# Kernel tuning notes

Hardware: AMD Instinct MI355X
Metric: run time of the kernel (lower is better)

Reference implementation:

```python
import jax, jax.numpy as jnp
import numpy as np

B, N, D_IN, E, H = 4, 512, 256, 64, 4
NEG = 1.0e9


def setup_inputs() -> dict:
    key = jax.random.key(0)
    ks = jax.random.split(key, 7)
    s = 1.0 / np.sqrt(D_IN)  # dense-init scale
    return {
        "x": jax.random.normal(ks[0], (B, N, D_IN), jnp.float32),
        "Wq": jax.random.normal(ks[1], (H, D_IN, E), jnp.float32) * s,
        "bq": jnp.zeros((H, E), jnp.float32),
        "Wk": jax.random.normal(ks[2], (H, D_IN, E), jnp.float32) * s,
        "bk": jnp.zeros((H, E), jnp.float32),
        "Wv": jax.random.normal(ks[3], (H, D_IN, E), jnp.float32) * s,
        "bv": jnp.zeros((H, E), jnp.float32),
    }


def _sdp(q, k, v):
    logits = jnp.einsum('bne,bme->bnm', q, k) / jnp.sqrt(jnp.asarray(E, q.dtype))
    return jnp.einsum('bnm,bme->bne', jax.nn.softmax(logits, axis=-1), v)


def _cosine(q, k, v):
    qn = q / jnp.linalg.norm(q, axis=-1, keepdims=True)
    kn = k / jnp.linalg.norm(k, axis=-1, keepdims=True)
    logits = jnp.einsum('bne,bme->bnm', qn, kn)
    return jnp.einsum('bnm,bme->bne', jax.nn.softmax(logits, axis=-1), v)


def _l1(q, k, v):
    # [B,N,N] L1 distances via broadcasted [B,N,N,E] diff, as in the original
    d = jnp.sum(jnp.abs(q[:, :, None, :] - k[:, None, :, :]), axis=-1)
    return jnp.einsum('bnm,bme->bne', jax.nn.softmax(-d, axis=-1), v)


def _l2(q, k, v):
    d = jnp.sqrt(jnp.sum(jnp.square(q[:, :, None, :] - k[:, None, :, :]), axis=-1))
    return jnp.einsum('bnm,bme->bne', jax.nn.softmax(-d, axis=-1), v)


_HEAD_FNS = (_sdp, _cosine, _l1, _l2)  # attention_types per head


def reference(x, Wq, bq, Wk, bk, Wv, bv):
    # Per-head projections: [B,H,N,E]
    q = jnp.einsum('bnd,hde->bhne', x, Wq) + bq[None, :, None, :]
    k = jnp.einsum('bnd,hde->bhne', x, Wk) + bk[None, :, None, :]
    v = jnp.einsum('bnd,hde->bhne', x, Wv) + bv[None, :, None, :]
    outs = [fn(q[:, h], k[:, h], v[:, h]) for h, fn in enumerate(_HEAD_FNS)]
    return jnp.concatenate(outs, axis=-1)  # [B,N,H*E]
```

## Files before the change

kernel.cpp:

```cpp
#include <hip/hip_runtime.h>
#include <hip/hip_bf16.h>
#include <math.h>

#define B_   4
#define N_   512
#define DIN  256
#define E_   64
#define H_   4

typedef __attribute__((ext_vector_type(8))) short bf16x8;
typedef __attribute__((ext_vector_type(4))) float f32x4;

__device__ __forceinline__ unsigned short f2bf(float f) {
    __hip_bfloat16 h = __float2bfloat16(f);
    return *reinterpret_cast<unsigned short*>(&h);
}

__global__ __launch_bounds__(256) void proj_kernel(
    const float* __restrict__ x,
    const float* __restrict__ Wq, const float* __restrict__ bq,
    const float* __restrict__ Wk, const float* __restrict__ bk,
    const float* __restrict__ Wv, const float* __restrict__ bv,
    float* __restrict__ Q, float* __restrict__ KT,
    float* __restrict__ qn2, float* __restrict__ kn2,
    unsigned short* __restrict__ Qp, unsigned short* __restrict__ Kp,
    unsigned short* __restrict__ VTp)
{
    const int tid = threadIdx.x;
    int blk = blockIdx.x;
    const int tile = blk & 15;  blk >>= 4;
    const int p    = blk % 3;   blk /= 3;
    const int h    = blk & 3;
    const int b    = blk >> 2;

    const float* W;
    const float* bias;
    if (p == 0)      { W = Wq; bias = bq; }
    else if (p == 1) { W = Wk; bias = bk; }
    else             { W = Wv; bias = bv; }
    W    += (size_t)h * DIN * E_;
    bias += h * E_;

    const int rowbase = tile * 32;
    const float* xb = x + ((size_t)b * N_ + rowbase) * DIN;

    __shared__ float XsT[64][34];
    __shared__ float Ws[64][64];
    __shared__ float Ys[64][33];

    const int tr = tid >> 4;
    const int tc = tid & 15;

    float acc[2][4];
    #pragma unroll
    for (int i = 0; i < 2; ++i)
        #pragma unroll
        for (int j = 0; j < 4; ++j) acc[i][j] = 0.f;

    for (int dc = 0; dc < DIN; dc += 64) {
        for (int l = tid; l < 2048; l += 256) {
            int r = l >> 6, d = l & 63;
            XsT[d][r] = xb[r * DIN + dc + d];
        }
        {
            const float4* Wg4 = (const float4*)(W + (size_t)dc * E_);
            #pragma unroll
            for (int i = 0; i < 4; ++i) ((float4*)Ws)[tid + i * 256] = Wg4[tid + i * 256];
        }
        __syncthreads();

        #pragma unroll 8
        for (int d = 0; d < 64; ++d) {
            float2 xv = *(const float2*)&XsT[d][tr * 2];
            float4 wv = *(const float4*)&Ws[d][tc * 4];
            acc[0][0] = fmaf(xv.x, wv.x, acc[0][0]);
            acc[0][1] = fmaf(xv.x, wv.y, acc[0][1]);
            acc[0][2] = fmaf(xv.x, wv.z, acc[0][2]);
            acc[0][3] = fmaf(xv.x, wv.w, acc[0][3]);
            acc[1][0] = fmaf(xv.y, wv.x, acc[1][0]);
            acc[1][1] = fmaf(xv.y, wv.y, acc[1][1]);
            acc[1][2] = fmaf(xv.y, wv.z, acc[1][2]);
            acc[1][3] = fmaf(xv.y, wv.w, acc[1][3]);
        }
        __syncthreads();
    }

    const size_t bh = (size_t)b * H_ + h;
    float4 bias4 = *(const float4*)&bias[tc * 4];
    float v0[4], v1[4];
    v0[0] = acc[0][0] + bias4.x; v0[1] = acc[0][1] + bias4.y;
    v0[2] = acc[0][2] + bias4.z; v0[3] = acc[0][3] + bias4.w;
    v1[0] = acc[1][0] + bias4.x; v1[1] = acc[1][1] + bias4.y;
    v1[2] = acc[1][2] + bias4.z; v1[3] = acc[1][3] + bias4.w;

    const int r0 = rowbase + tr * 2;

    if (p < 2) {
        float s0 = 0.f, s1 = 0.f;
        #pragma unroll
        for (int j = 0; j < 4; ++j) {
            s0 = fmaf(v0[j], v0[j], s0);
            s1 = fmaf(v1[j], v1[j], s1);
        }
        #pragma unroll
        for (int off = 1; off < 16; off <<= 1) {
            s0 += __shfl_xor(s0, off, 64);
            s1 += __shfl_xor(s1, off, 64);
        }
        if (tc == 0) {
            float* nrm = (p == 0) ? qn2 : kn2;
            nrm[bh * N_ + r0]     = s0;
            nrm[bh * N_ + r0 + 1] = s1;
        }
        unsigned short* pk = ((p == 0) ? Qp : Kp) + bh * (size_t)(N_ * E_);
        ushort4 u0, u1;
        u0.x = f2bf(v0[0]); u0.y = f2bf(v0[1]); u0.z = f2bf(v0[2]); u0.w = f2bf(v0[3]);
        u1.x = f2bf(v1[0]); u1.y = f2bf(v1[1]); u1.z = f2bf(v1[2]); u1.w = f2bf(v1[3]);
        *(ushort4*)&pk[(size_t)r0 * E_ + tc * 4]       = u0;
        *(ushort4*)&pk[(size_t)(r0 + 1) * E_ + tc * 4] = u1;
    }

    if (p == 0) {
        float* o = Q + bh * (size_t)(N_ * E_);
        *(float4*)&o[(size_t)r0 * E_ + tc * 4]       = make_float4(v0[0], v0[1], v0[2], v0[3]);
        *(float4*)&o[(size_t)(r0 + 1) * E_ + tc * 4] = make_float4(v1[0], v1[1], v1[2], v1[3]);
    } else {
        #pragma unroll
        for (int j = 0; j < 4; ++j) {
            Ys[tc * 4 + j][tr * 2]     = v0[j];
            Ys[tc * 4 + j][tr * 2 + 1] = v1[j];
        }
        __syncthreads();
        const int e  = tid >> 2;
        const int n0 = (tid & 3) * 8;
        if (p == 1) {
            float* o = KT + bh * (size_t)(E_ * N_) + (size_t)e * N_ + rowbase + n0;
            float4 a, c;
            a.x = Ys[e][n0 + 0]; a.y = Ys[e][n0 + 1];
            a.z = Ys[e][n0 + 2]; a.w = Ys[e][n0 + 3];
            c.x = Ys[e][n0 + 4]; c.y = Ys[e][n0 + 5];
            c.z = Ys[e][n0 + 6]; c.w = Ys[e][n0 + 7];
            *(float4*)&o[0] = a;
            *(float4*)&o[4] = c;
        } else {
            unsigned short* o = VTp + bh * (size_t)(E_ * N_) + (size_t)e * N_ + rowbase + n0;
            ushort4 a, c;
            a.x = f2bf(Ys[e][n0 + 0]); a.y = f2bf(Ys[e][n0 + 1]);
            a.z = f2bf(Ys[e][n0 + 2]); a.w = f2bf(Ys[e][n0 + 3]);
            c.x = f2bf(Ys[e][n0 + 4]); c.y = f2bf(Ys[e][n0 + 5]);
            c.z = f2bf(Ys[e][n0 + 6]); c.w = f2bf(Ys[e][n0 + 7]);
            *(ushort4*)&o[0] = a;
            *(ushort4*)&o[4] = c;
        }
    }
}

template <int HEAD>
__device__ __forceinline__ void mfma_logits(
    int w, int lane, size_t bh, int q0,
    const unsigned short* __restrict__ Qp,
    const unsigned short* __restrict__ Kp,
    const float* __restrict__ qn2, const float* __restrict__ kn2,
    char* Pw, float (*wmax)[16], float (*wsum)[16])
{
    const int g = lane >> 4, li = lane & 15;
    const int row0 = g * 4;
    const unsigned short* Qpb = Qp + bh * (N_ * E_) + (size_t)q0 * E_;
    const unsigned short* Kpb = Kp + bh * (N_ * E_);

    bf16x8 a0 = *(const bf16x8*)&Qpb[li * E_ + g * 8];
    bf16x8 a1 = *(const bf16x8*)&Qpb[li * E_ + g * 8 + 32];

    float qrow[4];
    if (HEAD == 1) {
        #pragma unroll
        for (int j = 0; j < 4; ++j) qrow[j] = rsqrtf(qn2[bh * N_ + q0 + row0 + j]);
    } else if (HEAD == 3) {
        #pragma unroll
        for (int j = 0; j < 4; ++j) qrow[j] = qn2[bh * N_ + q0 + row0 + j];
    }

    float lg[8][4];
    #pragma unroll
    for (int t = 0; t < 8; ++t) {
        const int m0 = w * 128 + t * 16;
        const unsigned short* kb = &Kpb[(size_t)(m0 + li) * E_ + g * 8];
        bf16x8 b0 = *(const bf16x8*)&kb[0];
        bf16x8 b1 = *(const bf16x8*)&kb[32];
        f32x4 acc = {0.f, 0.f, 0.f, 0.f};
        acc = __builtin_amdgcn_mfma_f32_16x16x32_bf16(a0, b0, acc, 0, 0, 0);
        acc = __builtin_amdgcn_mfma_f32_16x16x32_bf16(a1, b1, acc, 0, 0, 0);
        float kcol = 0.f, rk = 0.f;
        if (HEAD == 1) { kcol = kn2[bh * N_ + m0 + li]; rk = rsqrtf(kcol); }
        if (HEAD == 3) { kcol = kn2[bh * N_ + m0 + li]; }
        #pragma unroll
        for (int j = 0; j < 4; ++j) {
            float d = acc[j];
            if (HEAD == 0)      lg[t][j] = d * 0.125f;
            else if (HEAD == 1) lg[t][j] = d * qrow[j] * rk;
            else                lg[t][j] = -sqrtf(fmaxf(qrow[j] + kcol - 2.f * d, 0.f));
        }
    }

    float mx[4], gm[4];
    #pragma unroll
    for (int j = 0; j < 4; ++j) {
        float m = lg[0][j];
        #pragma unroll
        for (int t = 1; t < 8; ++t) m = fmaxf(m, lg[t][j]);
        #pragma unroll
        for (int off = 1; off < 16; off <<= 1) m = fmaxf(m, __shfl_xor(m, off, 64));
        mx[j] = m;
    }
    if (li == 0) {
        #pragma unroll
        for (int j = 0; j < 4; ++j) wmax[w][row0 + j] = mx[j];
    }
    __syncthreads();
    #pragma unroll
    for (int j = 0; j < 4; ++j)
        gm[j] = fmaxf(fmaxf(wmax[0][row0 + j], wmax[1][row0 + j]),
                      fmaxf(wmax[2][row0 + j], wmax[3][row0 + j]));

    float sm[4] = {0.f, 0.f, 0.f, 0.f};
    #pragma unroll
    for (int t = 0; t < 8; ++t) {
        #pragma unroll
        for (int j = 0; j < 4; ++j) {
            const int row = row0 + j;
            float pv = __expf(lg[t][j] - gm[j]);
            sm[j] += pv;
            const int byte = (row * 256 + (t * 16 + li) * 2) ^ ((row & 7) << 4);
            *(unsigned short*)(Pw + byte) = f2bf(pv);
        }
    }
    #pragma unroll
    for (int j = 0; j < 4; ++j) {
        float s = sm[j];
        #pragma unroll
        for (int off = 1; off < 16; off <<= 1) s += __shfl_xor(s, off, 64);
        if (li == 0) wsum[w][row0 + j] = s;
    }
}

__global__ __launch_bounds__(256) void attn_kernel(
    const float* __restrict__ Qf, const float* __restrict__ KT,
    const unsigned short* __restrict__ Qp, const unsigned short* __restrict__ Kp,
    const unsigned short* __restrict__ VTp,
    const float* __restrict__ qn2, const float* __restrict__ kn2,
    float* __restrict__ out)
{
    const int tid  = threadIdx.x;
    const int w    = tid >> 6;
    const int lane = tid & 63;
    int blk = blockIdx.x;
    const int qt = blk & 31;
    const int h  = (blk >> 5) & 3;
    const int b  = blk >> 7;
    const size_t bh = (size_t)b * H_ + h;
    const int q0 = qt * 16;

    __shared__ unsigned short Plds[4][2048];
    __shared__ float part[4][16][68];
    __shared__ float wmax[4][16];
    __shared__ float wsum[4][16];
    __shared__ float q_lds[16][72];

    const int g = lane >> 4, li = lane & 15;
    char* Pw = (char*)&Plds[w][0];

    if (h == 2) {
        {
            const int i4 = tid * 4;
            const int r = i4 >> 6, c = i4 & 63;
            *(float4*)&q_lds[r][c] =
                *(const float4*)&Qf[bh * (N_ * E_) + (size_t)(q0 + r) * E_ + c];
        }
        __syncthreads();

        float acc0[16], acc1[16];
        #pragma unroll
        for (int r = 0; r < 16; ++r) { acc0[r] = 0.f; acc1[r] = 0.f; }

        const float* kp = KT + bh * (E_ * N_) + w * 128 + 2 * lane;
        for (int c = 0; c < 4; ++c) {
            float2 kk[16];
            #pragma unroll
            for (int i = 0; i < 16; ++i) kk[i] = *(const float2*)&kp[(c * 16 + i) * N_];
            #pragma unroll
            for (int r = 0; r < 16; ++r) {
                const float* qr = &q_lds[r][c * 16];
                float4 qa = *(const float4*)&qr[0];
                float4 qb = *(const float4*)&qr[4];
                float4 qc = *(const float4*)&qr[8];
                float4 qd = *(const float4*)&qr[12];
                float qv[16] = {qa.x, qa.y, qa.z, qa.w, qb.x, qb.y, qb.z, qb.w,
                                qc.x, qc.y, qc.z, qc.w, qd.x, qd.y, qd.z, qd.w};
                #pragma unroll
                for (int i = 0; i < 16; ++i) {
                    acc0[r] += fabsf(kk[i].x - qv[i]);
                    acc1[r] += fabsf(kk[i].y - qv[i]);
                }
            }
        }

        #pragma unroll
        for (int r = 0; r < 16; ++r) {
            float mn = fminf(acc0[r], acc1[r]);
            #pragma unroll
            for (int off = 1; off < 64; off <<= 1) mn = fminf(mn, __shfl_xor(mn, off, 64));
            if (lane == 0) wmax[w][r] = mn;
        }
        __syncthreads();
        #pragma unroll
        for (int r = 0; r < 16; ++r) {
            float gmn = fminf(fminf(wmax[0][r], wmax[1][r]), fminf(wmax[2][r], wmax[3][r]));
            float p0 = __expf(gmn - acc0[r]);
            float p1 = __expf(gmn - acc1[r]);
            float s = p0 + p1;
            #pragma unroll
            for (int off = 1; off < 64; off <<= 1) s += __shfl_xor(s, off, 64);
            if (lane == 0) wsum[w][r] = s;
            unsigned int pk = (unsigned int)f2bf(p0) | ((unsigned int)f2bf(p1) << 16);
            const int byte = (r * 256 + lane * 4) ^ ((r & 7) << 4);
            *(unsigned int*)(Pw + byte) = pk;
        }
    } else if (h == 0) {
        mfma_logits<0>(w, lane, bh, q0, Qp, Kp, qn2, kn2, Pw, wmax, wsum);
    } else if (h == 1) {
        mfma_logits<1>(w, lane, bh, q0, Qp, Kp, qn2, kn2, Pw, wmax, wsum);
    } else {
        mfma_logits<3>(w, lane, bh, q0, Qp, Kp, qn2, kn2, Pw, wmax, wsum);
    }

    {
        bf16x8 pa[4];
        #pragma unroll
        for (int s = 0; s < 4; ++s) {
            const int byte = (li * 256 + (s * 32 + g * 8) * 2) ^ ((li & 7) << 4);
            pa[s] = *(const bf16x8*)(Pw + byte);
        }
        const unsigned short* Vb = VTp + bh * (E_ * N_);
        const int row0 = g * 4;
        #pragma unroll
        for (int et = 0; et < 4; ++et) {
            f32x4 acc = {0.f, 0.f, 0.f, 0.f};
            #pragma unroll
            for (int s = 0; s < 4; ++s) {
                bf16x8 vb = *(const bf16x8*)&Vb[(size_t)(et * 16 + li) * N_
                                                + w * 128 + s * 32 + g * 8];
                acc = __builtin_amdgcn_mfma_f32_16x16x32_bf16(pa[s], vb, acc, 0, 0, 0);
            }
            #pragma unroll
            for (int j = 0; j < 4; ++j) part[w][row0 + j][et * 16 + li] = acc[j];
        }
    }
    __syncthreads();

    #pragma unroll
    for (int k = 0; k < 4; ++k) {
        const int idx = tid + k * 256;
        const int row = idx >> 6, e = idx & 63;
        float s = part[0][row][e] + part[1][row][e] + part[2][row][e] + part[3][row][e];
        float rs = wsum[0][row] + wsum[1][row] + wsum[2][row] + wsum[3][row];
        out[((size_t)b * N_ + q0 + row) * (H_ * E_) + h * E_ + e] = s / rs;
    }
}

extern "C" void kernel_launch(void* const* d_in, const int* in_sizes, int n_in,
                              void* d_out, int out_size, void* d_ws, size_t ws_size,
                              hipStream_t stream)
{
    const float* x  = (const float*)d_in[0];
    const float* Wq = (const float*)d_in[1];
    const float* bq = (const float*)d_in[2];
    const float* Wk = (const float*)d_in[3];
    const float* bk = (const float*)d_in[4];
    const float* Wv = (const float*)d_in[5];
    const float* bv = (const float*)d_in[6];
    float* out = (float*)d_out;

    const size_t qkv = (size_t)B_ * H_ * N_ * E_;
    float* Q   = (float*)d_ws;
    float* KT  = Q + qkv;
    float* qn2 = KT + qkv;
    float* kn2 = qn2 + (size_t)B_ * H_ * N_;
    unsigned short* Qp  = (unsigned short*)(kn2 + (size_t)B_ * H_ * N_);
    unsigned short* Kp  = Qp + qkv;
    unsigned short* VTp = Kp + qkv;

    proj_kernel<<<B_ * H_ * 3 * (N_ / 32), 256, 0, stream>>>(
        x, Wq, bq, Wk, bk, Wv, bv, Q, KT, qn2, kn2, Qp, Kp, VTp);
    attn_kernel<<<B_ * H_ * (N_ / 16), 256, 0, stream>>>(
        Q, KT, Qp, Kp, VTp, qn2, kn2, out);
}
```

Baseline: 58.97 us.

## Double attention block to eight waves with shared P tile and split PV

The attention kernel now runs 512 threads per block, eight waves, each handling 64 keys instead of 128. The probability tile is stored as one shared 16x512 LDS buffer instead of per-wave slices. The PV product is redistributed so each wave computes one 16-column output tile over half the keys, which cuts the cross-wave reduction to two partials. This halves per-thread work on the L1 head and the logits, aiming to shorten the critical path and hide latency. The cost is an extra block-wide barrier and more LDS per block, which may lower occupancy.

```diff
diff --git a/kernel.cpp b/kernel.cpp
--- a/kernel.cpp
+++ b/kernel.cpp
@@ -155,13 +155,15 @@
     }
 }
 
+#define PROW 1024
+
 template <int HEAD>
 __device__ __forceinline__ void mfma_logits(
     int w, int lane, size_t bh, int q0,
     const unsigned short* __restrict__ Qp,
     const unsigned short* __restrict__ Kp,
     const float* __restrict__ qn2, const float* __restrict__ kn2,
-    char* Pw, float (*wmax)[16], float (*wsum)[16])
+    char* Pb, float (*wmax)[16], float (*wsum)[16])
 {
     const int g = lane >> 4, li = lane & 15;
     const int row0 = g * 4;
@@ -180,10 +182,10 @@
         for (int j = 0; j < 4; ++j) qrow[j] = qn2[bh * N_ + q0 + row0 + j];
     }
 
-    float lg[8][4];
-    #pragma unroll
-    for (int t = 0; t < 8; ++t) {
-        const int m0 = w * 128 + t * 16;
+    float lg[4][4];
+    #pragma unroll
+    for (int t = 0; t < 4; ++t) {
+        const int m0 = w * 64 + t * 16;
         const unsigned short* kb = &Kpb[(size_t)(m0 + li) * E_ + g * 8];
         bf16x8 b0 = *(const bf16x8*)&kb[0];
         bf16x8 b1 = *(const bf16x8*)&kb[32];
@@ -202,12 +204,12 @@
         }
     }
 
-    float mx[4], gm[4];
+    float mx[4];
     #pragma unroll
     for (int j = 0; j < 4; ++j) {
         float m = lg[0][j];
         #pragma unroll
-        for (int t = 1; t < 8; ++t) m = fmaxf(m, lg[t][j]);
+        for (int t = 1; t < 4; ++t) m = fmaxf(m, lg[t][j]);
         #pragma unroll
         for (int off = 1; off < 16; off <<= 1) m = fmaxf(m, __shfl_xor(m, off, 64));
         mx[j] = m;
@@ -217,21 +219,27 @@
         for (int j = 0; j < 4; ++j) wmax[w][row0 + j] = mx[j];
     }
     __syncthreads();
-    #pragma unroll
-    for (int j = 0; j < 4; ++j)
-        gm[j] = fmaxf(fmaxf(wmax[0][row0 + j], wmax[1][row0 + j]),
-                      fmaxf(wmax[2][row0 + j], wmax[3][row0 + j]));
+
+    float gm[4];
+    #pragma unroll
+    for (int j = 0; j < 4; ++j) {
+        float m = wmax[0][row0 + j];
+        #pragma unroll
+        for (int ww = 1; ww < 8; ++ww) m = fmaxf(m, wmax[ww][row0 + j]);
+        gm[j] = m;
+    }
 
     float sm[4] = {0.f, 0.f, 0.f, 0.f};
     #pragma unroll
-    for (int t = 0; t < 8; ++t) {
+    for (int t = 0; t < 4; ++t) {
         #pragma unroll
         for (int j = 0; j < 4; ++j) {
             const int row = row0 + j;
+            const int key = w * 64 + t * 16 + li;
             float pv = __expf(lg[t][j] - gm[j]);
             sm[j] += pv;
-            const int byte = (row * 256 + (t * 16 + li) * 2) ^ ((row & 7) << 4);
-            *(unsigned short*)(Pw + byte) = f2bf(pv);
+            const int byte = (row * PROW + key * 2) ^ ((row & 7) << 4);
+            *(unsigned short*)(Pb + byte) = f2bf(pv);
         }
     }
     #pragma unroll
@@ -243,7 +251,7 @@
     }
 }
 
-__global__ __launch_bounds__(256) void attn_kernel(
+__global__ __launch_bounds__(512) void attn_kernel(
     const float* __restrict__ Qf, const float* __restrict__ KT,
     const unsigned short* __restrict__ Qp, const unsigned short* __restrict__ Kp,
     const unsigned short* __restrict__ VTp,
@@ -260,33 +268,34 @@
     const size_t bh = (size_t)b * H_ + h;
     const int q0 = qt * 16;
 
-    __shared__ unsigned short Plds[4][2048];
-    __shared__ float part[4][16][68];
-    __shared__ float wmax[4][16];
-    __shared__ float wsum[4][16];
+    __shared__ unsigned short Plds[16 * 512];
+    __shared__ float part[2][16][68];
+    __shared__ float wmax[8][16];
+    __shared__ float wsum[8][16];
     __shared__ float q_lds[16][72];
 
     const int g = lane >> 4, li = lane & 15;
-    char* Pw = (char*)&Plds[w][0];
+    char* Pb = (char*)Plds;
 
     if (h == 2) {
-        {
-            const int i4 = tid * 4;
-            const int r = i4 >> 6, c = i4 & 63;
+        if (tid < 256) {
+            const int r = tid >> 4, c = (tid & 15) * 4;
             *(float4*)&q_lds[r][c] =
                 *(const float4*)&Qf[bh * (N_ * E_) + (size_t)(q0 + r) * E_ + c];
         }
         __syncthreads();
 
-        float acc0[16], acc1[16];
-        #pragma unroll
-        for (int r = 0; r < 16; ++r) { acc0[r] = 0.f; acc1[r] = 0.f; }
-
-        const float* kp = KT + bh * (E_ * N_) + w * 128 + 2 * lane;
+        const int n = w * 64 + lane;
+        const float* kp = KT + bh * (E_ * N_) + n;
+        float acc[16];
+        #pragma unroll
+        for (int r = 0; r < 16; ++r) acc[r] = 0.f;
+
+        #pragma unroll
         for (int c = 0; c < 4; ++c) {
-            float2 kk[16];
-            #pragma unroll
-            for (int i = 0; i < 16; ++i) kk[i] = *(const float2*)&kp[(c * 16 + i) * N_];
+            float kk[16];
+            #pragma unroll
+            for (int i = 0; i < 16; ++i) kk[i] = kp[(size_t)(c * 16 + i) * N_];
             #pragma unroll
             for (int r = 0; r < 16; ++r) {
                 const float* qr = &q_lds[r][c * 16];
@@ -297,72 +306,67 @@
                 float qv[16] = {qa.x, qa.y, qa.z, qa.w, qb.x, qb.y, qb.z, qb.w,
                                 qc.x, qc.y, qc.z, qc.w, qd.x, qd.y, qd.z, qd.w};
                 #pragma unroll
-                for (int i = 0; i < 16; ++i) {
-                    acc0[r] += fabsf(kk[i].x - qv[i]);
-                    acc1[r] += fabsf(kk[i].y - qv[i]);
-                }
+                for (int i = 0; i < 16; ++i) acc[r] += fabsf(kk[i] - qv[i]);
             }
         }
 
         #pragma unroll
         for (int r = 0; r < 16; ++r) {
-            float mn = fminf(acc0[r], acc1[r]);
+            float mn = acc[r];
             #pragma unroll
             for (int off = 1; off < 64; off <<= 1) mn = fminf(mn, __shfl_xor(mn, off, 64));
             if (lane == 0) wmax[w][r] = mn;
         }
         __syncthreads();
+
         #pragma unroll
         for (int r = 0; r < 16; ++r) {
-            float gmn = fminf(fminf(wmax[0][r], wmax[1][r]), fminf(wmax[2][r], wmax[3][r]));
-            float p0 = __expf(gmn - acc0[r]);
-            float p1 = __expf(gmn - acc1[r]);
-            float s = p0 + p1;
+            float gmn = wmax[0][r];
+            #pragma unroll
+            for (int ww = 1; ww < 8; ++ww) gmn = fminf(gmn, wmax[ww][r]);
+            float p = __expf(gmn - acc[r]);
+            float s = p;
             #pragma unroll
             for (int off = 1; off < 64; off <<= 1) s += __shfl_xor(s, off, 64);
             if (lane == 0) wsum[w][r] = s;
-            unsigned int pk = (unsigned int)f2bf(p0) | ((unsigned int)f2bf(p1) << 16);
-            const int byte = (r * 256 + lane * 4) ^ ((r & 7) << 4);
-            *(unsigned int*)(Pw + byte) = pk;
+            const int byte = (r * PROW + n * 2) ^ ((r & 7) << 4);
+            *(unsigned short*)(Pb + byte) = f2bf(p);
         }
     } else if (h == 0) {
-        mfma_logits<0>(w, lane, bh, q0, Qp, Kp, qn2, kn2, Pw, wmax, wsum);
+        mfma_logits<0>(w, lane, bh, q0, Qp, Kp, qn2, kn2, Pb, wmax, wsum);
     } else if (h == 1) {
-        mfma_logits<1>(w, lane, bh, q0, Qp, Kp, qn2, kn2, Pw, wmax, wsum);
+        mfma_logits<1>(w, lane, bh, q0, Qp, Kp, qn2, kn2, Pb, wmax, wsum);
     } else {
-        mfma_logits<3>(w, lane, bh, q0, Qp, Kp, qn2, kn2, Pw, wmax, wsum);
-    }
+        mfma_logits<3>(w, lane, bh, q0, Qp, Kp, qn2, kn2, Pb, wmax, wsum);
+    }
+    __syncthreads();
 
     {
-        bf16x8 pa[4];
-        #pragma unroll
-        for (int s = 0; s < 4; ++s) {
-            const int byte = (li * 256 + (s * 32 + g * 8) * 2) ^ ((li & 7) << 4);
-            pa[s] = *(const bf16x8*)(Pw + byte);
-        }
-        const unsigned short* Vb = VTp + bh * (E_ * N_);
-        const int row0 = g * 4;
-        #pragma unroll
-        for (int et = 0; et < 4; ++et) {
-            f32x4 acc = {0.f, 0.f, 0.f, 0.f};
-            #pragma unroll
-            for (int s = 0; s < 4; ++s) {
-                bf16x8 vb = *(const bf16x8*)&Vb[(size_t)(et * 16 + li) * N_
-                                                + w * 128 + s * 32 + g * 8];
-                acc = __builtin_amdgcn_mfma_f32_16x16x32_bf16(pa[s], vb, acc, 0, 0, 0);
-            }
-            #pragma unroll
-            for (int j = 0; j < 4; ++j) part[w][row0 + j][et * 16 + li] = acc[j];
-        }
+        const int et = w & 3, kh = w >> 2;
+        f32x4 acc = {0.f, 0.f, 0.f, 0.f};
+        const unsigned short* Vb = VTp + bh * (E_ * N_)
+                                 + (size_t)(et * 16 + li) * N_ + kh * 256;
+        #pragma unroll
+        for (int s = 0; s < 8; ++s) {
+            const int byte = (li * PROW + (kh * 256 + s * 32 + g * 8) * 2)
+                           ^ ((li & 7) << 4);
+            bf16x8 pa = *(const bf16x8*)(Pb + byte);
+            bf16x8 vb = *(const bf16x8*)&Vb[s * 32 + g * 8];
+            acc = __builtin_amdgcn_mfma_f32_16x16x32_bf16(pa, vb, acc, 0, 0, 0);
+        }
+        #pragma unroll
+        for (int j = 0; j < 4; ++j) part[kh][g * 4 + j][et * 16 + li] = acc[j];
     }
     __syncthreads();
 
     #pragma unroll
-    for (int k = 0; k < 4; ++k) {
-        const int idx = tid + k * 256;
+    for (int k = 0; k < 2; ++k) {
+        const int idx = tid + k * 512;
         const int row = idx >> 6, e = idx & 63;
-        float s = part[0][row][e] + part[1][row][e] + part[2][row][e] + part[3][row][e];
-        float rs = wsum[0][row] + wsum[1][row] + wsum[2][row] + wsum[3][row];
+        float s = part[0][row][e] + part[1][row][e];
+        float rs = 0.f;
+        #pragma unroll
+        for (int ww = 0; ww < 8; ++ww) rs += wsum[ww][row];
         out[((size_t)b * N_ + q0 + row) * (H_ * E_) + h * E_ + e] = s / rs;
     }
 }
@@ -391,6 +395,6 @@
 
     proj_kernel<<<B_ * H_ * 3 * (N_ / 32), 256, 0, stream>>>(
         x, Wq, bq, Wk, bk, Wv, bv, Q, KT, qn2, kn2, Qp, Kp, VTp);
-    attn_kernel<<<B_ * H_ * (N_ / 16), 256, 0, stream>>>(
+    attn_kernel<<<B_ * H_ * (N_ / 16), 512, 0, stream>>>(
         Q, KT, Qp, Kp, VTp, qn2, kn2, out);
 }
```

New measurement: 188.0 us. 3.19x slower.

## Store bf16 Q/K/V in MFMA fragment-major layout for coalesced operand loads

Applied to the files above, without the earlier changes.

The projection kernel now writes the bf16 Q, K and V copies in a pre-swizzled layout. Each 16-lane group's 8-element MFMA operand fragment sits contiguously, so a wavefront's operand load becomes one contiguous 1 KB read instead of strided row reads. V goes through a new small LDS staging tile so it can be repacked into this fragment order. The attention kernel's index math changes to match. The cost is extra LDS traffic and more complex indexing in the projection kernel.

```diff
diff --git a/kernel.cpp b/kernel.cpp
--- a/kernel.cpp
+++ b/kernel.cpp
@@ -9,6 +9,7 @@
 #define H_   4
 
 typedef __attribute__((ext_vector_type(8))) short bf16x8;
+typedef __attribute__((ext_vector_type(8))) unsigned short u16x8;
 typedef __attribute__((ext_vector_type(4))) float f32x4;
 
 __device__ __forceinline__ unsigned short f2bf(float f) {
@@ -23,8 +24,8 @@
     const float* __restrict__ Wv, const float* __restrict__ bv,
     float* __restrict__ Q, float* __restrict__ KT,
     float* __restrict__ qn2, float* __restrict__ kn2,
-    unsigned short* __restrict__ Qp, unsigned short* __restrict__ Kp,
-    unsigned short* __restrict__ VTp)
+    unsigned short* __restrict__ QF, unsigned short* __restrict__ KF,
+    unsigned short* __restrict__ VF)
 {
     const int tid = threadIdx.x;
     int blk = blockIdx.x;
@@ -47,6 +48,7 @@
     __shared__ float XsT[64][34];
     __shared__ float Ws[64][64];
     __shared__ float Ys[64][33];
+    __shared__ unsigned short Vst[64][40];
 
     const int tr = tid >> 4;
     const int tc = tid & 15;
@@ -112,19 +114,21 @@
             nrm[bh * N_ + r0]     = s0;
             nrm[bh * N_ + r0 + 1] = s1;
         }
-        unsigned short* pk = ((p == 0) ? Qp : Kp) + bh * (size_t)(N_ * E_);
+        unsigned short* f = ((p == 0) ? QF : KF) + bh * (size_t)(N_ * E_);
+        const int t_ = r0 >> 4, li = r0 & 15;
+        const int gg = tc >> 1, j0 = (tc & 1) * 4;
         ushort4 u0, u1;
         u0.x = f2bf(v0[0]); u0.y = f2bf(v0[1]); u0.z = f2bf(v0[2]); u0.w = f2bf(v0[3]);
         u1.x = f2bf(v1[0]); u1.y = f2bf(v1[1]); u1.z = f2bf(v1[2]); u1.w = f2bf(v1[3]);
-        *(ushort4*)&pk[(size_t)r0 * E_ + tc * 4]       = u0;
-        *(ushort4*)&pk[(size_t)(r0 + 1) * E_ + tc * 4] = u1;
+        *(ushort4*)&f[(size_t)((t_ * 8 + gg) * 16 + li) * 8 + j0]       = u0;
+        *(ushort4*)&f[(size_t)((t_ * 8 + gg) * 16 + li + 1) * 8 + j0]   = u1;
     }
 
     if (p == 0) {
         float* o = Q + bh * (size_t)(N_ * E_);
         *(float4*)&o[(size_t)r0 * E_ + tc * 4]       = make_float4(v0[0], v0[1], v0[2], v0[3]);
         *(float4*)&o[(size_t)(r0 + 1) * E_ + tc * 4] = make_float4(v1[0], v1[1], v1[2], v1[3]);
-    } else {
+    } else if (p == 1) {
         #pragma unroll
         for (int j = 0; j < 4; ++j) {
             Ys[tc * 4 + j][tr * 2]     = v0[j];
@@ -133,43 +137,47 @@
         __syncthreads();
         const int e  = tid >> 2;
         const int n0 = (tid & 3) * 8;
-        if (p == 1) {
-            float* o = KT + bh * (size_t)(E_ * N_) + (size_t)e * N_ + rowbase + n0;
-            float4 a, c;
-            a.x = Ys[e][n0 + 0]; a.y = Ys[e][n0 + 1];
-            a.z = Ys[e][n0 + 2]; a.w = Ys[e][n0 + 3];
-            c.x = Ys[e][n0 + 4]; c.y = Ys[e][n0 + 5];
-            c.z = Ys[e][n0 + 6]; c.w = Ys[e][n0 + 7];
-            *(float4*)&o[0] = a;
-            *(float4*)&o[4] = c;
-        } else {
-            unsigned short* o = VTp + bh * (size_t)(E_ * N_) + (size_t)e * N_ + rowbase + n0;
-            ushort4 a, c;
-            a.x = f2bf(Ys[e][n0 + 0]); a.y = f2bf(Ys[e][n0 + 1]);
-            a.z = f2bf(Ys[e][n0 + 2]); a.w = f2bf(Ys[e][n0 + 3]);
-            c.x = f2bf(Ys[e][n0 + 4]); c.y = f2bf(Ys[e][n0 + 5]);
-            c.z = f2bf(Ys[e][n0 + 6]); c.w = f2bf(Ys[e][n0 + 7]);
-            *(ushort4*)&o[0] = a;
-            *(ushort4*)&o[4] = c;
-        }
+        float* o = KT + bh * (size_t)(E_ * N_) + (size_t)e * N_ + rowbase + n0;
+        float4 a, c;
+        a.x = Ys[e][n0 + 0]; a.y = Ys[e][n0 + 1];
+        a.z = Ys[e][n0 + 2]; a.w = Ys[e][n0 + 3];
+        c.x = Ys[e][n0 + 4]; c.y = Ys[e][n0 + 5];
+        c.z = Ys[e][n0 + 6]; c.w = Ys[e][n0 + 7];
+        *(float4*)&o[0] = a;
+        *(float4*)&o[4] = c;
+    } else {
+        #pragma unroll
+        for (int j = 0; j < 4; ++j) {
+            Vst[tc * 4 + j][tr * 2]     = f2bf(v0[j]);
+            Vst[tc * 4 + j][tr * 2 + 1] = f2bf(v1[j]);
+        }
+        __syncthreads();
+        const int et = tid >> 6, rem = tid & 63;
+        const int g = rem >> 4, li = rem & 15;
+        const int e = et * 16 + li, kb = rowbase >> 5;
+        u16x8 wv8;
+        #pragma unroll
+        for (int j = 0; j < 8; ++j) wv8[j] = Vst[e][g * 8 + j];
+        *(u16x8*)&VF[bh * (size_t)(N_ * E_)
+                     + (size_t)(((et * 16 + kb) * 4 + g) * 16 + li) * 8] = wv8;
     }
 }
 
 template <int HEAD>
 __device__ __forceinline__ void mfma_logits(
-    int w, int lane, size_t bh, int q0,
-    const unsigned short* __restrict__ Qp,
-    const unsigned short* __restrict__ Kp,
+    int w, int lane, size_t bh, int qt, int q0,
+    const unsigned short* __restrict__ QF,
+    const unsigned short* __restrict__ KF,
     const float* __restrict__ qn2, const float* __restrict__ kn2,
     char* Pw, float (*wmax)[16], float (*wsum)[16])
 {
     const int g = lane >> 4, li = lane & 15;
     const int row0 = g * 4;
-    const unsigned short* Qpb = Qp + bh * (N_ * E_) + (size_t)q0 * E_;
-    const unsigned short* Kpb = Kp + bh * (N_ * E_);
-
-    bf16x8 a0 = *(const bf16x8*)&Qpb[li * E_ + g * 8];
-    bf16x8 a1 = *(const bf16x8*)&Qpb[li * E_ + g * 8 + 32];
+    const unsigned short* qfb = QF + bh * (N_ * E_) + (size_t)qt * 1024;
+    const unsigned short* kfb = KF + bh * (N_ * E_);
+
+    bf16x8 a0 = *(const bf16x8*)&qfb[(g * 16 + li) * 8];
+    bf16x8 a1 = *(const bf16x8*)&qfb[((g + 4) * 16 + li) * 8];
 
     float qrow[4];
     if (HEAD == 1) {
@@ -183,10 +191,10 @@
     float lg[8][4];
     #pragma unroll
     for (int t = 0; t < 8; ++t) {
-        const int m0 = w * 128 + t * 16;
-        const unsigned short* kb = &Kpb[(size_t)(m0 + li) * E_ + g * 8];
-        bf16x8 b0 = *(const bf16x8*)&kb[0];
-        bf16x8 b1 = *(const bf16x8*)&kb[32];
+        const int kt = w * 8 + t;
+        const int m0 = kt * 16;
+        bf16x8 b0 = *(const bf16x8*)&kfb[(size_t)((kt * 8 + g) * 16 + li) * 8];
+        bf16x8 b1 = *(const bf16x8*)&kfb[(size_t)((kt * 8 + g + 4) * 16 + li) * 8];
         f32x4 acc = {0.f, 0.f, 0.f, 0.f};
         acc = __builtin_amdgcn_mfma_f32_16x16x32_bf16(a0, b0, acc, 0, 0, 0);
         acc = __builtin_amdgcn_mfma_f32_16x16x32_bf16(a1, b1, acc, 0, 0, 0);
@@ -245,8 +253,8 @@
 
 __global__ __launch_bounds__(256) void attn_kernel(
     const float* __restrict__ Qf, const float* __restrict__ KT,
-    const unsigned short* __restrict__ Qp, const unsigned short* __restrict__ Kp,
-    const unsigned short* __restrict__ VTp,
+    const unsigned short* __restrict__ QF, const unsigned short* __restrict__ KF,
+    const unsigned short* __restrict__ VF,
     const float* __restrict__ qn2, const float* __restrict__ kn2,
     float* __restrict__ out)
 {
@@ -326,11 +334,11 @@
             *(unsigned int*)(Pw + byte) = pk;
         }
     } else if (h == 0) {
-        mfma_logits<0>(w, lane, bh, q0, Qp, Kp, qn2, kn2, Pw, wmax, wsum);
+        mfma_logits<0>(w, lane, bh, qt, q0, QF, KF, qn2, kn2, Pw, wmax, wsum);
     } else if (h == 1) {
-        mfma_logits<1>(w, lane, bh, q0, Qp, Kp, qn2, kn2, Pw, wmax, wsum);
+        mfma_logits<1>(w, lane, bh, qt, q0, QF, KF, qn2, kn2, Pw, wmax, wsum);
     } else {
-        mfma_logits<3>(w, lane, bh, q0, Qp, Kp, qn2, kn2, Pw, wmax, wsum);
+        mfma_logits<3>(w, lane, bh, qt, q0, QF, KF, qn2, kn2, Pw, wmax, wsum);
     }
 
     {
@@ -340,15 +348,15 @@
             const int byte = (li * 256 + (s * 32 + g * 8) * 2) ^ ((li & 7) << 4);
             pa[s] = *(const bf16x8*)(Pw + byte);
         }
-        const unsigned short* Vb = VTp + bh * (E_ * N_);
+        const unsigned short* vfb = VF + bh * (N_ * E_);
         const int row0 = g * 4;
         #pragma unroll
         for (int et = 0; et < 4; ++et) {
             f32x4 acc = {0.f, 0.f, 0.f, 0.f};
             #pragma unroll
             for (int s = 0; s < 4; ++s) {
-                bf16x8 vb = *(const bf16x8*)&Vb[(size_t)(et * 16 + li) * N_
-                                                + w * 128 + s * 32 + g * 8];
+                bf16x8 vb = *(const bf16x8*)&vfb[
+                    (size_t)(((et * 16 + w * 4 + s) * 4 + g) * 16 + li) * 8];
                 acc = __builtin_amdgcn_mfma_f32_16x16x32_bf16(pa[s], vb, acc, 0, 0, 0);
             }
             #pragma unroll
@@ -385,12 +393,12 @@
     float* KT  = Q + qkv;
     float* qn2 = KT + qkv;
     float* kn2 = qn2 + (size_t)B_ * H_ * N_;
-    unsigned short* Qp  = (unsigned short*)(kn2 + (size_t)B_ * H_ * N_);
-    unsigned short* Kp  = Qp + qkv;
-    unsigned short* VTp = Kp + qkv;
+    unsigned short* QF = (unsigned short*)(kn2 + (size_t)B_ * H_ * N_);
+    unsigned short* KF = QF + qkv;
+    unsigned short* VF = KF + qkv;
 
     proj_kernel<<<B_ * H_ * 3 * (N_ / 32), 256, 0, stream>>>(
-        x, Wq, bq, Wk, bk, Wv, bv, Q, KT, qn2, kn2, Qp, Kp, VTp);
+        x, Wq, bq, Wk, bk, Wv, bv, Q, KT, qn2, kn2, QF, KF, VF);
     attn_kernel<<<B_ * H_ * (N_ / 16), 256, 0, stream>>>(
-        Q, KT, Qp, Kp, VTp, qn2, kn2, out);
+        Q, KT, QF, KF, VF, qn2, kn2, out);
 }
```

Result: faster. 57.79 us (-2.0%).
